# Performance work log

Hardware: AMD Instinct MI355X
Metric: run time of the kernel (lower is better)

The kernel has to match this reference:

```python
import jax, jax.numpy as jnp
import numpy as np


def _warp3d(img, flow):
    """Faithful port of Warper3d.forward.

    img:  [B, C, D, H, W]
    flow: [B, 3, D, H, W]  (flow[:,0]=x/W disp, flow[:,1]=y/H disp, flow[:,2]=z/D disp)

    The torch module normalizes coords align_corners=True style (2*v/(S-1)-1)
    but calls F.grid_sample with its DEFAULT align_corners=False and
    padding_mode='border'. We replicate exactly that composition.
    """
    B, C, D, H, W = img.shape
    dt = img.dtype
    zz = jnp.arange(D, dtype=dt).reshape(1, D, 1, 1)
    yy = jnp.arange(H, dtype=dt).reshape(1, 1, H, 1)
    xx = jnp.arange(W, dtype=dt).reshape(1, 1, 1, W)

    vx = xx + flow[:, 0]  # [B,D,H,W]
    vy = yy + flow[:, 1]
    vz = zz + flow[:, 2]

    # module's normalization (align_corners=True convention)
    gx = 2.0 * vx / (W - 1) - 1.0
    gy = 2.0 * vy / (H - 1) - 1.0
    gz = 2.0 * vz / (D - 1) - 1.0

    # grid_sample default align_corners=False un-normalization
    ix = ((gx + 1.0) * W - 1.0) * 0.5
    iy = ((gy + 1.0) * H - 1.0) * 0.5
    iz = ((gz + 1.0) * D - 1.0) * 0.5

    # padding_mode='border': clamp sample coords into the volume
    ix = jnp.clip(ix, 0.0, W - 1)
    iy = jnp.clip(iy, 0.0, H - 1)
    iz = jnp.clip(iz, 0.0, D - 1)

    x0f = jnp.floor(ix); wx = ix - x0f
    y0f = jnp.floor(iy); wy = iy - y0f
    z0f = jnp.floor(iz); wz = iz - z0f

    x0 = x0f.astype(jnp.int32); x1 = jnp.clip(x0 + 1, 0, W - 1)
    y0 = y0f.astype(jnp.int32); y1 = jnp.clip(y0 + 1, 0, H - 1)
    z0 = z0f.astype(jnp.int32); z1 = jnp.clip(z0 + 1, 0, D - 1)

    img_flat = img.reshape(B, C, D * H * W)

    def gather(zc, yc, xc):
        idx = (zc * H + yc) * W + xc            # [B,D,H,W]
        v = jnp.take_along_axis(img_flat, idx.reshape(B, 1, -1), axis=2)
        return v.reshape(B, C, D, H, W)

    wx = wx[:, None]; wy = wy[:, None]; wz = wz[:, None]  # [B,1,D,H,W]

    out = (
        gather(z0, y0, x0) * (1 - wz) * (1 - wy) * (1 - wx)
        + gather(z0, y0, x1) * (1 - wz) * (1 - wy) * wx
        + gather(z0, y1, x0) * (1 - wz) * wy * (1 - wx)
        + gather(z0, y1, x1) * (1 - wz) * wy * wx
        + gather(z1, y0, x0) * wz * (1 - wy) * (1 - wx)
        + gather(z1, y0, x1) * wz * (1 - wy) * wx
        + gather(z1, y1, x0) * wz * wy * (1 - wx)
        + gather(z1, y1, x1) * wz * wy * wx
    )
    return out


def setup_inputs() -> dict:
    key = jax.random.key(0)
    k1, k2 = jax.random.split(key)
    B, D, H, W = 4, 64, 192, 192
    img = jax.random.normal(k1, (B, 1, D, H, W), dtype=jnp.float32)
    flow = jax.random.normal(k2, (B, 3, D, H, W), dtype=jnp.float32)
    return {"img": img, "flow": flow}


def reference(img, flow):
    return _warp3d(img, flow)
```

## Files before the change

kernel.cpp:

```cpp
#include <hip/hip_runtime.h>

#define B_  4
#define D_  64
#define H_  192
#define W_  192
#define HW_ (H_ * W_)
#define DHW_ (D_ * H_ * W_)
#define NTOT (B_ * DHW_)

#define TY 8
#define TZ 2
#define SY (TY + 8)
#define SZ (TZ + 8)
#define SPLANE (SY * W_)
#define SLDS (SZ * SPLANE)
#define TILE_OUT (W_ * TY * TZ)
#define VEC 4
#define TPB (TILE_OUT / VEC)
#define NWG_Y (H_ / TY)
#define NWG_Z (D_ / TZ)
#define NWG (B_ * NWG_Z * NWG_Y)

typedef float f4 __attribute__((ext_vector_type(4)));
typedef float f2 __attribute__((ext_vector_type(2)));
typedef f2 f2u __attribute__((aligned(4)));

__global__ __launch_bounds__(TPB, 1) void warp3d_kernel(
    const float* __restrict__ img,
    const float* __restrict__ flow,
    float* __restrict__ out)
{
    __shared__ float lds[SLDS];

    int wg = blockIdx.x;
    int b  = wg / (NWG_Z * NWG_Y);
    int rr = wg - b * (NWG_Z * NWG_Y);
    int tz = rr / NWG_Y;
    int Z  = tz * TZ;
    int Y  = (rr - tz * NWG_Y) * TY;
    int Zs = min(max(Z - 4, 0), D_ - SZ);
    int Ys = min(max(Y - 4, 0), H_ - SY);

    const float* im = img + (size_t)b * DHW_;
    int t = threadIdx.x;

    {
        int yy = (t * 4) / W_;
        int xs = (t * 4) - yy * W_;
        const float* src = im + (Ys + yy) * W_ + xs;
#pragma unroll
        for (int j = 0; j < SZ; ++j) {
            f4 v = *(const f4*)(src + (size_t)(Zs + j) * HW_);
            *(f4*)(lds + j * SPLANE + t * 4) = v;
        }
    }
    __syncthreads();

    int o  = t * VEC;
    int x  = o % W_;
    int q  = o / W_;
    int yi = q % TY;
    int zi = q / TY;
    int y  = Y + yi;
    int z  = Z + zi;

    size_t nbase = (size_t)b * DHW_ + ((size_t)z * H_ + y) * W_ + x;
    const float* fl = flow + (size_t)b * 3 * DHW_ + ((size_t)z * H_ + y) * W_ + x;
    f4 fx = __builtin_nontemporal_load((const f4*)fl);
    f4 fy = __builtin_nontemporal_load((const f4*)(fl + DHW_));
    f4 fz = __builtin_nontemporal_load((const f4*)(fl + 2 * DHW_));

    const float sx = (float)W_ / (float)(W_ - 1);
    const float sy = (float)H_ / (float)(H_ - 1);
    const float sz = (float)D_ / (float)(D_ - 1);

    int   xb[VEC], y0a[VEC], z0a[VEC], hi[VEC], val[VEC];
    float wxv[VEC], wyv[VEC], wzv[VEC];

#pragma unroll
    for (int i = 0; i < VEC; ++i) {
        float ix = ((float)(x + i) + fx[i]) * sx - 0.5f;
        float iy = ((float)y + fy[i]) * sy - 0.5f;
        float iz = ((float)z + fz[i]) * sz - 0.5f;
        ix = fminf(fmaxf(ix, 0.0f), (float)(W_ - 1));
        iy = fminf(fmaxf(iy, 0.0f), (float)(H_ - 1));
        iz = fminf(fmaxf(iz, 0.0f), (float)(D_ - 1));

        float x0f = floorf(ix), y0f = floorf(iy), z0f = floorf(iz);
        wxv[i] = ix - x0f;
        wyv[i] = iy - y0f;
        wzv[i] = iz - z0f;

        int x0 = (int)x0f, y0 = (int)y0f, z0 = (int)z0f;
        int xbi = min(x0, W_ - 2);
        xb[i] = xbi;
        hi[i] = x0 - xbi;
        y0a[i] = y0;
        z0a[i] = z0;
        int y1 = min(y0 + 1, H_ - 1);
        int z1 = min(z0 + 1, D_ - 1);
        val[i] = (y0 >= Ys) & (y1 <= Ys + SY - 1) &
                 (z0 >= Zs) & (z1 <= Zs + SZ - 1);
    }

    f4 res;
#pragma unroll
    for (int i = 0; i < VEC; ++i) {
        int y0 = y0a[i], z0 = z0a[i];
        int y1 = min(y0 + 1, H_ - 1);
        int z1 = min(z0 + 1, D_ - 1);
        float v000, v001, v010, v011, v100, v101, v110, v111;
        if (val[i]) {
            int i00 = ((z0 - Zs) * SY + (y0 - Ys)) * W_ + xb[i];
            int i01 = ((z0 - Zs) * SY + (y1 - Ys)) * W_ + xb[i];
            int i10 = ((z1 - Zs) * SY + (y0 - Ys)) * W_ + xb[i];
            int i11 = ((z1 - Zs) * SY + (y1 - Ys)) * W_ + xb[i];
            v000 = lds[i00]; v001 = lds[i00 + 1];
            v010 = lds[i01]; v011 = lds[i01 + 1];
            v100 = lds[i10]; v101 = lds[i10 + 1];
            v110 = lds[i11]; v111 = lds[i11 + 1];
        } else {
            f2 p00 = *(const f2u*)(im + (z0 * H_ + y0) * W_ + xb[i]);
            f2 p01 = *(const f2u*)(im + (z0 * H_ + y1) * W_ + xb[i]);
            f2 p10 = *(const f2u*)(im + (z1 * H_ + y0) * W_ + xb[i]);
            f2 p11 = *(const f2u*)(im + (z1 * H_ + y1) * W_ + xb[i]);
            v000 = p00.x; v001 = p00.y;
            v010 = p01.x; v011 = p01.y;
            v100 = p10.x; v101 = p10.y;
            v110 = p11.x; v111 = p11.y;
        }
        if (hi[i]) { v000 = v001; v010 = v011; v100 = v101; v110 = v111; }

        float wx = wxv[i], wy = wyv[i], wz = wzv[i];
        float c00 = v000 + wx * (v001 - v000);
        float c01 = v010 + wx * (v011 - v010);
        float c10 = v100 + wx * (v101 - v100);
        float c11 = v110 + wx * (v111 - v110);
        float c0 = c00 + wy * (c01 - c00);
        float c1 = c10 + wy * (c11 - c10);
        res[i] = c0 + wz * (c1 - c0);
    }
    __builtin_nontemporal_store(res, (f4*)(out + nbase));
}

extern "C" void kernel_launch(void* const* d_in, const int* in_sizes, int n_in,
                              void* d_out, int out_size, void* d_ws, size_t ws_size,
                              hipStream_t stream) {
    const float* img  = (const float*)d_in[0];
    const float* flow = (const float*)d_in[1];
    float* out = (float*)d_out;

    warp3d_kernel<<<NWG, TPB, 0, stream>>>(img, flow, out);
}
```

Before: 216.0 us.

## Use single-z-slice tiles with a smaller LDS halo for higher occupancy

Each workgroup now produces one z-plane of 8 rows instead of two z-planes. It stages an 8x13-row LDS halo (about 80 KB, down from about 123 KB), uses 2 outputs per thread, and raises the launch bounds to allow several waves per SIMD. The aim is more resident workgroups for hiding gather and global-load latency. The cost is more redundant halo loading per output and a strided cooperative load loop. Samples that fall outside the smaller halo take the slower global-memory fallback path more often.

Result: slower. 222.7 us (+3.1%).

```diff
diff --git a/kernel.cpp b/kernel.cpp
--- a/kernel.cpp
+++ b/kernel.cpp
@@ -6,26 +6,25 @@
 #define W_  192
 #define HW_ (H_ * W_)
 #define DHW_ (D_ * H_ * W_)
-#define NTOT (B_ * DHW_)
 
+#define VEC 2
 #define TY 8
-#define TZ 2
-#define SY (TY + 8)
-#define SZ (TZ + 8)
+#define SY 13
+#define SZ 8
 #define SPLANE (SY * W_)
 #define SLDS (SZ * SPLANE)
-#define TILE_OUT (W_ * TY * TZ)
-#define VEC 4
+#define TILE_OUT (W_ * TY)
 #define TPB (TILE_OUT / VEC)
 #define NWG_Y (H_ / TY)
-#define NWG_Z (D_ / TZ)
-#define NWG (B_ * NWG_Z * NWG_Y)
+#define NWG (B_ * D_ * NWG_Y)
+#define CPLANE (SPLANE / 4)
+#define NCHUNK (SLDS / 4)
 
 typedef float f4 __attribute__((ext_vector_type(4)));
 typedef float f2 __attribute__((ext_vector_type(2)));
 typedef f2 f2u __attribute__((aligned(4)));
 
-__global__ __launch_bounds__(TPB, 1) void warp3d_kernel(
+__global__ __launch_bounds__(TPB, 6) void warp3d_kernel(
     const float* __restrict__ img,
     const float* __restrict__ flow,
     float* __restrict__ out)
@@ -33,105 +32,86 @@
     __shared__ float lds[SLDS];
 
     int wg = blockIdx.x;
-    int b  = wg / (NWG_Z * NWG_Y);
-    int rr = wg - b * (NWG_Z * NWG_Y);
-    int tz = rr / NWG_Y;
-    int Z  = tz * TZ;
-    int Y  = (rr - tz * NWG_Y) * TY;
-    int Zs = min(max(Z - 4, 0), D_ - SZ);
-    int Ys = min(max(Y - 4, 0), H_ - SY);
+    int b  = wg / (D_ * NWG_Y);
+    int rr = wg - b * (D_ * NWG_Y);
+    int z  = rr / NWG_Y;
+    int Y  = (rr - z * NWG_Y) * TY;
+
+    int Zs = min(max(z - 3, 0), D_ - SZ);
+    int Ys = min(max(Y - 2, 0), H_ - SY);
 
     const float* im = img + (size_t)b * DHW_;
     int t = threadIdx.x;
 
     {
-        int yy = (t * 4) / W_;
-        int xs = (t * 4) - yy * W_;
-        const float* src = im + (Ys + yy) * W_ + xs;
-#pragma unroll
-        for (int j = 0; j < SZ; ++j) {
-            f4 v = *(const f4*)(src + (size_t)(Zs + j) * HW_);
-            *(f4*)(lds + j * SPLANE + t * 4) = v;
+        const float* src = im + Ys * W_;
+        for (int idx = t; idx < NCHUNK; idx += TPB) {
+            int j   = idx / CPLANE;
+            int rem = idx - j * CPLANE;
+            f4 v = *(const f4*)(src + (size_t)(Zs + j) * HW_ + rem * 4);
+            *(f4*)(lds + j * SPLANE + rem * 4) = v;
         }
     }
     __syncthreads();
 
     int o  = t * VEC;
     int x  = o % W_;
-    int q  = o / W_;
-    int yi = q % TY;
-    int zi = q / TY;
-    int y  = Y + yi;
-    int z  = Z + zi;
+    int y  = Y + o / W_;
 
     size_t nbase = (size_t)b * DHW_ + ((size_t)z * H_ + y) * W_ + x;
     const float* fl = flow + (size_t)b * 3 * DHW_ + ((size_t)z * H_ + y) * W_ + x;
-    f4 fx = __builtin_nontemporal_load((const f4*)fl);
-    f4 fy = __builtin_nontemporal_load((const f4*)(fl + DHW_));
-    f4 fz = __builtin_nontemporal_load((const f4*)(fl + 2 * DHW_));
+    f2 fx = __builtin_nontemporal_load((const f2u*)fl);
+    f2 fy = __builtin_nontemporal_load((const f2u*)(fl + DHW_));
+    f2 fz = __builtin_nontemporal_load((const f2u*)(fl + 2 * DHW_));
 
-    const float sx = (float)W_ / (float)(W_ - 1);
-    const float sy = (float)H_ / (float)(H_ - 1);
-    const float sz = (float)D_ / (float)(D_ - 1);
+    const float sxc = (float)W_ / (float)(W_ - 1);
+    const float syc = (float)H_ / (float)(H_ - 1);
+    const float szc = (float)D_ / (float)(D_ - 1);
 
-    int   xb[VEC], y0a[VEC], z0a[VEC], hi[VEC], val[VEC];
-    float wxv[VEC], wyv[VEC], wzv[VEC];
-
+    f2 res;
 #pragma unroll
     for (int i = 0; i < VEC; ++i) {
-        float ix = ((float)(x + i) + fx[i]) * sx - 0.5f;
-        float iy = ((float)y + fy[i]) * sy - 0.5f;
-        float iz = ((float)z + fz[i]) * sz - 0.5f;
+        float ix = ((float)(x + i) + fx[i]) * sxc - 0.5f;
+        float iy = ((float)y + fy[i]) * syc - 0.5f;
+        float iz = ((float)z + fz[i]) * szc - 0.5f;
         ix = fminf(fmaxf(ix, 0.0f), (float)(W_ - 1));
         iy = fminf(fmaxf(iy, 0.0f), (float)(H_ - 1));
         iz = fminf(fmaxf(iz, 0.0f), (float)(D_ - 1));
 
         float x0f = floorf(ix), y0f = floorf(iy), z0f = floorf(iz);
-        wxv[i] = ix - x0f;
-        wyv[i] = iy - y0f;
-        wzv[i] = iz - z0f;
+        float wx = ix - x0f, wy = iy - y0f, wz = iz - z0f;
 
         int x0 = (int)x0f, y0 = (int)y0f, z0 = (int)z0f;
-        int xbi = min(x0, W_ - 2);
-        xb[i] = xbi;
-        hi[i] = x0 - xbi;
-        y0a[i] = y0;
-        z0a[i] = z0;
+        int xb = min(x0, W_ - 2);
+        int hi = x0 - xb;
         int y1 = min(y0 + 1, H_ - 1);
         int z1 = min(z0 + 1, D_ - 1);
-        val[i] = (y0 >= Ys) & (y1 <= Ys + SY - 1) &
-                 (z0 >= Zs) & (z1 <= Zs + SZ - 1);
-    }
 
-    f4 res;
-#pragma unroll
-    for (int i = 0; i < VEC; ++i) {
-        int y0 = y0a[i], z0 = z0a[i];
-        int y1 = min(y0 + 1, H_ - 1);
-        int z1 = min(z0 + 1, D_ - 1);
+        bool val = (y0 >= Ys) & (y1 <= Ys + SY - 1) &
+                   (z0 >= Zs) & (z1 <= Zs + SZ - 1);
+
         float v000, v001, v010, v011, v100, v101, v110, v111;
-        if (val[i]) {
-            int i00 = ((z0 - Zs) * SY + (y0 - Ys)) * W_ + xb[i];
-            int i01 = ((z0 - Zs) * SY + (y1 - Ys)) * W_ + xb[i];
-            int i10 = ((z1 - Zs) * SY + (y0 - Ys)) * W_ + xb[i];
-            int i11 = ((z1 - Zs) * SY + (y1 - Ys)) * W_ + xb[i];
+        if (val) {
+            int i00 = ((z0 - Zs) * SY + (y0 - Ys)) * W_ + xb;
+            int i01 = ((z0 - Zs) * SY + (y1 - Ys)) * W_ + xb;
+            int i10 = ((z1 - Zs) * SY + (y0 - Ys)) * W_ + xb;
+            int i11 = ((z1 - Zs) * SY + (y1 - Ys)) * W_ + xb;
             v000 = lds[i00]; v001 = lds[i00 + 1];
             v010 = lds[i01]; v011 = lds[i01 + 1];
             v100 = lds[i10]; v101 = lds[i10 + 1];
             v110 = lds[i11]; v111 = lds[i11 + 1];
         } else {
-            f2 p00 = *(const f2u*)(im + (z0 * H_ + y0) * W_ + xb[i]);
-            f2 p01 = *(const f2u*)(im + (z0 * H_ + y1) * W_ + xb[i]);
-            f2 p10 = *(const f2u*)(im + (z1 * H_ + y0) * W_ + xb[i]);
-            f2 p11 = *(const f2u*)(im + (z1 * H_ + y1) * W_ + xb[i]);
+            f2 p00 = *(const f2u*)(im + (z0 * H_ + y0) * W_ + xb);
+            f2 p01 = *(const f2u*)(im + (z0 * H_ + y1) * W_ + xb);
+            f2 p10 = *(const f2u*)(im + (z1 * H_ + y0) * W_ + xb);
+            f2 p11 = *(const f2u*)(im + (z1 * H_ + y1) * W_ + xb);
             v000 = p00.x; v001 = p00.y;
             v010 = p01.x; v011 = p01.y;
             v100 = p10.x; v101 = p10.y;
             v110 = p11.x; v111 = p11.y;
         }
-        if (hi[i]) { v000 = v001; v010 = v011; v100 = v101; v110 = v111; }
+        if (hi) { v000 = v001; v010 = v011; v100 = v101; v110 = v111; }
 
-        float wx = wxv[i], wy = wyv[i], wz = wzv[i];
         float c00 = v000 + wx * (v001 - v000);
         float c01 = v010 + wx * (v011 - v010);
         float c10 = v100 + wx * (v101 - v100);
@@ -140,7 +120,7 @@
         float c1 = c10 + wy * (c11 - c10);
         res[i] = c0 + wz * (c1 - c0);
     }
-    __builtin_nontemporal_store(res, (f4*)(out + nbase));
+    __builtin_nontemporal_store(res, (f2*)(out + nbase));
 }
 
 extern "C" void kernel_launch(void* const* d_in, const int* in_sizes, int n_in,
```
